# Performance work log

Hardware: AMD Instinct MI355X
Metric: run time of the kernel (lower is better)

Reference implementation:

```python
import jax, jax.numpy as jnp
import numpy as np

PS = 32768        # bag size (num patches)
D_IN = 1024       # input feature dim (hardcoded Linear(1024,512))
D = 512           # mlp_dim
D_ATT = 128       # DAttention hidden dim (ABMIL D)
N_CLS = 2
MASK_RATIO_H = 0.5
K_MASK = int(np.ceil(PS * MASK_RATIO_H))   # high-attention patches masked out
LEN_KEEP = PS - K_MASK                     # static keep length


def setup_inputs() -> dict:
    key = jax.random.key(0)
    ks = jax.random.split(key, 8)
    n = lambda i, shp, sc: jax.random.normal(ks[i], shp, dtype=jnp.float32) * sc
    return {
        "x": n(0, (1, PS, D_IN), 1.0),
        "attn": jax.random.uniform(ks[1], (1, PS), dtype=jnp.float32),
        "teacher_cls_feat": n(2, (1, D), 1.0),
        # patch_to_emb: Linear(1024,512) + ReLU (xavier-ish init)
        "W_emb": n(3, (D_IN, D), 0.03), "b_emb": jnp.zeros((D,), jnp.float32),
        # DAttention score net: Linear(512,128) -> GELU -> Linear(128,1)
        "W_a1": n(4, (D, D_ATT), 0.06), "b_a1": jnp.zeros((D_ATT,), jnp.float32),
        "W_a2": n(5, (D_ATT, 1), 0.12), "b_a2": jnp.zeros((1,), jnp.float32),
        # predictor: Linear(512, n_classes)
        "W_pred": n(6, (D, N_CLS), 0.06), "b_pred": jnp.zeros((N_CLS,), jnp.float32),
    }


def _keep_ids(attn_1d):
    # select_mask_fn(largest=True, mask_ratio=0.5, random_ratio=1.0, select_inv=False):
    # top-k highest-attention indices are MASKED; keep = set-difference complement.
    _, top_idx = jax.lax.top_k(attn_1d, K_MASK)
    masked = jnp.zeros((PS,), dtype=bool).at[top_idx].set(True)
    # complement in ascending order (matches set(range(ps)).difference iteration)
    return jnp.nonzero(~masked, size=LEN_KEEP, fill_value=0)[0]


def reference(x, attn, teacher_cls_feat, W_emb, b_emb, W_a1, b_a1, W_a2, b_a2,
              W_pred, b_pred):
    # patch_to_emb + ReLU  (dropout=0 -> identity)
    h = jax.nn.relu(jnp.einsum("bnd,de->bne", x, W_emb) + b_emb)   # [1,PS,512]

    keep = _keep_ids(attn[0])                                        # [LEN_KEEP]
    hk = h[:, keep, :]                                               # [1,LK,512]

    # DAttention pooling: scores -> softmax over kept instances -> weighted sum
    s = jax.nn.gelu(jnp.einsum("bnd,dk->bnk", hk, W_a1) + b_a1, approximate=False)
    s = (jnp.einsum("bnk,ko->bno", s, W_a2) + b_a2)[..., 0]          # [1,LK]
    A = jax.nn.softmax(s, axis=-1)
    feat = jnp.einsum("bn,bnd->bd", A, hk)                           # [1,512]

    logit = feat @ W_pred + b_pred                                   # [1,2]

    # SoftTargetCrossEntropy_v2 between student bag feature and (detached) teacher
    t = jax.lax.stop_gradient(teacher_cls_feat)
    cls_loss = jnp.mean(jnp.sum(
        -jax.nn.softmax(t, axis=-1) * jax.nn.log_softmax(feat, axis=-1), axis=-1))

    return logit, cls_loss
```

## Files before the change

### kernel.cpp

```cpp
#include <hip/hip_runtime.h>
#include <hip/hip_bf16.h>
#include <math.h>

#define PS    32768
#define DIN   1024
#define DMID  512
#define DATT  128
#define KMASK 16384
#define LKEEP 16384

typedef unsigned short u16;
typedef __attribute__((ext_vector_type(8))) short short8;
typedef __attribute__((ext_vector_type(4))) float f32x4;

__device__ __forceinline__ u16 f2bf(float f){
  unsigned x = __float_as_uint(f);
  unsigned r = (x + 0x7fffu + ((x >> 16) & 1u)) >> 16;
  return (u16)r;
}
__device__ __forceinline__ u16 f2bf_hw(float f){
  __hip_bfloat16 h = __float2bfloat16(f);
  return *reinterpret_cast<u16*>(&h);
}
__device__ __forceinline__ float bf2f(u16 u){
  return __uint_as_float(((unsigned)u) << 16);
}
__device__ __forceinline__ unsigned fkey(float f){
  unsigned b = __float_as_uint(f);
  return (b & 0x80000000u) ? ~b : (b | 0x80000000u);
}

#define GLDS16(g,l) __builtin_amdgcn_global_load_lds( \
    (const __attribute__((address_space(1))) void*)(g), \
    (__attribute__((address_space(3))) void*)(l), 16, 0, 0)

#define MEMPIN() asm volatile("" ::: "memory")

__global__ __launch_bounds__(1024) void k_head(const float* __restrict__ attn,
                                               int* __restrict__ keep_ids,
                                               const float* __restrict__ Wemb,
                                               u16* __restrict__ wet,
                                               const float* __restrict__ Wa1,
                                               u16* __restrict__ wa1t){
  __shared__ int histL[16384];
  __shared__ int suf[1024];
  __shared__ unsigned ck[4096];
  __shared__ int ci[4096];
  __shared__ float tile[4][32][33];
  __shared__ int sh_B, sh_kp, cnt;
  __shared__ unsigned sh_C;
  __shared__ int sh_thr;
  __shared__ int wbase[16];
  __shared__ int sh_base;
  const int t = threadIdx.x, b = blockIdx.x;

  if (b >= 32){
    const int grp = t >> 8, ts = t & 255;
    const int ob = (b - 32) * 4 + grp;
    const int tx = ts & 31, ty = ts >> 5;
    if (ob < 512){
      const int c0 = (ob & 15) * 32, r0 = (ob >> 4) * 32;
      for (int i = 0; i < 32; i += 8)
        tile[grp][ty + i][tx] = Wemb[(size_t)(r0 + ty + i) * DMID + c0 + tx];
      __syncthreads();
      for (int i = 0; i < 32; i += 8)
        wet[(size_t)(c0 + ty + i) * DIN + r0 + tx] = f2bf(tile[grp][tx][ty + i]);
    } else {
      const int b2 = ob - 512;
      const int c0 = (b2 & 3) * 32, r0 = (b2 >> 2) * 32;
      for (int i = 0; i < 32; i += 8)
        tile[grp][ty + i][tx] = Wa1[(size_t)(r0 + ty + i) * DATT + c0 + tx];
      __syncthreads();
      for (int i = 0; i < 32; i += 8)
        wa1t[(size_t)(c0 + ty + i) * DMID + r0 + tx] = f2bf(tile[grp][tx][ty + i]);
    }
    return;
  }

  for (int i = t; i < 16384; i += 1024) histL[i] = 0;
  __syncthreads();
  for (int i = t; i < PS; i += 1024)
    atomicAdd(&histL[fkey(attn[i]) >> 18], 1);
  __syncthreads();

  int local[16]; int s = 0;
  const int base = t * 16;
  for (int j = 0; j < 16; j++){ local[j] = histL[base + j]; s += local[j]; }
  suf[t] = s; __syncthreads();
  for (int off = 1; off < 1024; off <<= 1){
    int v = (t + off < 1024) ? suf[t + off] : 0;
    __syncthreads();
    suf[t] += v;
    __syncthreads();
  }
  const int above = (t < 1023) ? suf[t + 1] : 0;
  if (above < KMASK && KMASK <= suf[t]){
    int cum = above;
    for (int bb = 15; bb >= 0; bb--){
      int c = local[bb];
      if (cum + c >= KMASK){ sh_B = base + bb; sh_kp = KMASK - cum; break; }
      cum += c;
    }
  }
  if (t == 0) cnt = 0;
  __syncthreads();
  const unsigned B = (unsigned)sh_B;
  const int kp = sh_kp;

  for (int i = t; i < PS; i += 1024){
    unsigned u = fkey(attn[i]);
    if ((u >> 18) == B){
      int p = atomicAdd(&cnt, 1);
      if (p < 4096){ ck[p] = u; ci[p] = i; }
    }
  }
  __syncthreads();
  int n = cnt; if (n > 4096) n = 4096;
  for (int p = t; p < n; p += 1024){
    const unsigned mk = ck[p]; const int mi = ci[p];
    int rank = 0;
    for (int j = 0; j < n; j++){
      const unsigned kj = ck[j];
      rank += (kj > mk) || (kj == mk && ci[j] < mi);
    }
    if (rank == kp - 1){ sh_C = mk; sh_thr = mi; }
  }
  __syncthreads();
  const unsigned C = sh_C;
  const int thr = sh_thr;

  const int i = b * 1024 + t;
  const unsigned u = fkey(attn[i]);
  const bool kept = (u < C) || (u == C && i > thr);
  const unsigned long long bal = __ballot(kept);
  const int lane = t & 63, w = t >> 6;
  if (lane == 0) wbase[w] = __popcll(bal);
  int cnt2 = 0;
  for (int j = t; j < b * 1024; j += 1024){
    const unsigned u2 = fkey(attn[j]);
    cnt2 += (u2 < C) || (u2 == C && j > thr);
  }
  suf[t] = cnt2; __syncthreads();
  for (int st = 512; st > 0; st >>= 1){ if (t < st) suf[t] += suf[t + st]; __syncthreads(); }
  if (t == 0){
    sh_base = suf[0];
    int run = 0;
    for (int j = 0; j < 16; j++){ int c = wbase[j]; wbase[j] = run; run += c; }
  }
  __syncthreads();
  if (kept){
    const int lr = __popcll(bal & ((1ull << lane) - 1ull));
    keep_ids[sh_base + wbase[w] + lr] = i;
  }
}

__global__ __launch_bounds__(512) void k_gemm1g(const float* __restrict__ xg,
                                                const int* __restrict__ keep,
                                                const u16* __restrict__ wet,
                                                const float* __restrict__ bemb,
                                                u16* __restrict__ hbf){
  __shared__ __align__(16) u16 As[2][128 * 32];
  __shared__ __align__(16) u16 Bs[2][128 * 32];
  const int t = threadIdx.x;
  const int wid = t >> 6, lane = t & 63;
  const int g = lane >> 4, li = lane & 15;
  const int m_ = blockIdx.x;
  const int by = (m_ & 7) + 8 * (m_ >> 5);
  const int bx = (m_ >> 3) & 3;
  const int brow = by * 128, bcol = bx * 128;
  const int wrow0 = (wid >> 2) * 64, wcol0 = (wid & 3) * 32;

  f32x4 acc[4][2];
  for (int mm = 0; mm < 4; mm++)
    for (int nn = 0; nn < 2; nn++)
      acc[mm][nn] = (f32x4){0.f, 0.f, 0.f, 0.f};

  const int rsub = t >> 2, q8 = (t & 3) * 8;
  const float* gA = xg + (size_t)keep[brow + rsub] * DIN + q8;
  const int r4 = lane >> 2, cB = lane & 3;
  const u16* gB = wet + ((size_t)(bcol + wid * 16 + r4) * DIN + cB * 8);

#define CVT_STORE(dstbuf, lo, hi) { \
    short8 pk_; \
    pk_[0] = (short)f2bf_hw((lo).x); pk_[1] = (short)f2bf_hw((lo).y); \
    pk_[2] = (short)f2bf_hw((lo).z); pk_[3] = (short)f2bf_hw((lo).w); \
    pk_[4] = (short)f2bf_hw((hi).x); pk_[5] = (short)f2bf_hw((hi).y); \
    pk_[6] = (short)f2bf_hw((hi).z); pk_[7] = (short)f2bf_hw((hi).w); \
    *(short8*)&As[dstbuf][rsub * 32 + q8] = pk_; }

#define READ_MFMA(cur) { \
    short8 a_[4], b_[2]; \
    _Pragma("unroll") \
    for (int mm = 0; mm < 4; mm++) \
      a_[mm] = *(const short8*)&As[cur][(wrow0 + mm * 16 + li) * 32 + g * 8]; \
    _Pragma("unroll") \
    for (int nn = 0; nn < 2; nn++) \
      b_[nn] = *(const short8*)&Bs[cur][(wcol0 + nn * 16 + li) * 32 + g * 8]; \
    for (int mm = 0; mm < 4; mm++) \
      for (int nn = 0; nn < 2; nn++) \
        acc[mm][nn] = __builtin_amdgcn_mfma_f32_16x16x32_bf16(a_[mm], b_[nn], acc[mm][nn], 0, 0, 0); }

  float4 a0lo = *(const float4*)(gA);
  float4 a0hi = *(const float4*)(gA + 4);
  MEMPIN();
  GLDS16(gB, &Bs[0][wid * 512]);
  MEMPIN();
  float4 avlo = *(const float4*)(gA + 32);
  float4 avhi = *(const float4*)(gA + 36);
  MEMPIN();
  CVT_STORE(0, a0lo, a0hi);
  asm volatile("s_waitcnt vmcnt(2) lgkmcnt(0)" ::: "memory");
  __builtin_amdgcn_s_barrier();

#pragma unroll 2
  for (int k = 0; k < 30; k++){
    const int cur = k & 1, nxt = cur ^ 1;
    GLDS16(gB + (k + 1) * 32, &Bs[nxt][wid * 512]);
    MEMPIN();
    float4 nvlo = *(const float4*)(gA + (k + 2) * 32);
    float4 nvhi = *(const float4*)(gA + (k + 2) * 32 + 4);
    asm volatile("s_waitcnt vmcnt(5)" ::: "memory");
    READ_MFMA(cur);
    MEMPIN();
    CVT_STORE(nxt, avlo, avhi);
    avlo = nvlo; avhi = nvhi;
    asm volatile("s_waitcnt lgkmcnt(0)" ::: "memory");
    __builtin_amdgcn_s_barrier();
  }
  {
    GLDS16(gB + 31 * 32, &Bs[1][wid * 512]);
    asm volatile("s_waitcnt vmcnt(3)" ::: "memory");
    READ_MFMA(0);
    MEMPIN();
    CVT_STORE(1, avlo, avhi);
    asm volatile("s_waitcnt lgkmcnt(0)" ::: "memory");
    __builtin_amdgcn_s_barrier();
  }
  {
    asm volatile("s_waitcnt vmcnt(0)" ::: "memory");
    READ_MFMA(1);
  }
#undef CVT_STORE
#undef READ_MFMA

  for (int nn = 0; nn < 2; nn++){
    const int col = bcol + wcol0 + nn * 16 + li;
    const float be = bemb[col];
    for (int mm = 0; mm < 4; mm++){
      const int row0 = brow + wrow0 + mm * 16 + g * 4;
      f32x4 v = acc[mm][nn];
      for (int r = 0; r < 4; r++){
        float val = v[r] + be;
        if (val < 0.f) val = 0.f;
        hbf[(size_t)(row0 + r) * DMID + col] = f2bf(val);
      }
    }
  }
}

__global__ __launch_bounds__(256) void k_gemm2(const u16* __restrict__ hbf,
                                               const u16* __restrict__ wa1t,
                                               const float* __restrict__ ba1,
                                               const float* __restrict__ wa2,
                                               const float* __restrict__ ba2,
                                               float* __restrict__ s_out,
                                               float* __restrict__ smax,
                                               float* __restrict__ ssum,
                                               float* __restrict__ partial){
  __shared__ __align__(16) u16 As[64 * 32];
  __shared__ __align__(16) u16 Bs[128 * 32];
  __shared__ float p_lds[64];
  __shared__ float sh_m;
  const int t = threadIdx.x;
  const int wid = t >> 6, lane = t & 63;
  const int g = lane >> 4, li = lane & 15;
  const int brow = blockIdx.x * 64;
  const int wrow0 = (wid >> 1) * 32, wcol0 = (wid & 1) * 64;

  f32x4 acc[2][4];
  for (int m = 0; m < 2; m++)
    for (int n = 0; n < 4; n++)
      acc[m][n] = (f32x4){0.f, 0.f, 0.f, 0.f};

  const int r4 = lane >> 2, c4 = lane & 3;
  const u16* gA = hbf  + ((size_t)(brow + wid * 16 + r4) * DMID + c4 * 8);
  const u16* gB = wa1t + ((size_t)(wid * 32 + r4) * DMID + c4 * 8);
  u16* lA = As + wid * 512;
  u16* lB = Bs + wid * 1024;

  for (int k0 = 0; k0 < DMID; k0 += 32){
    GLDS16(gA + k0,             lA);
    GLDS16(gB + k0,             lB);
    GLDS16(gB + 16 * DMID + k0, lB + 512);
    __syncthreads();
    short8 a[2], b[4];
    for (int m = 0; m < 2; m++)
      a[m] = *(const short8*)&As[(wrow0 + m * 16 + li) * 32 + g * 8];
    for (int n = 0; n < 4; n++)
      b[n] = *(const short8*)&Bs[(wcol0 + n * 16 + li) * 32 + g * 8];
    for (int m = 0; m < 2; m++)
      for (int n = 0; n < 4; n++)
        acc[m][n] = __builtin_amdgcn_mfma_f32_16x16x32_bf16(a[m], b[n], acc[m][n], 0, 0, 0);
    __syncthreads();
  }

  float rsum[2][4] = {{0.f,0.f,0.f,0.f},{0.f,0.f,0.f,0.f}};
  for (int n = 0; n < 4; n++){
    const int col = wcol0 + n * 16 + li;
    const float b1 = ba1[col], w2 = wa2[col];
    for (int m = 0; m < 2; m++){
      f32x4 v = acc[m][n];
      for (int r = 0; r < 4; r++){
        float xv = v[r] + b1;
        float ge = 0.5f * xv * (1.0f + erff(xv * 0.70710678118654752f));
        rsum[m][r] += ge * w2;
      }
    }
  }
  const float bb = ba2[0];
  for (int m = 0; m < 2; m++){
    for (int r = 0; r < 4; r++){
      float v = rsum[m][r];
      v += __shfl_xor(v, 1); v += __shfl_xor(v, 2);
      v += __shfl_xor(v, 4); v += __shfl_xor(v, 8);
      if (li == 0) s_out[brow + wrow0 + m * 16 + g * 4 + r] = v + bb;
    }
  }
  __syncthreads();
  if (t < 64){
    const float sv = s_out[brow + t];
    float mx = sv;
    for (int off = 1; off < 64; off <<= 1) mx = fmaxf(mx, __shfl_xor(mx, off));
    float ez = expf(sv - mx);
    for (int off = 1; off < 64; off <<= 1) ez += __shfl_xor(ez, off);
    if (t == 0){ smax[blockIdx.x] = mx; ssum[blockIdx.x] = ez; sh_m = mx; }
  }
  __syncthreads();
  if (t < 64) p_lds[t] = expf(s_out[brow + t] - sh_m);
  __syncthreads();
  {
    const int d0 = t * 2;
    float v0 = 0.f, v1 = 0.f;
    for (int j = 0; j < 64; j++){
      const float pj = p_lds[j];
      const unsigned hv = *(const unsigned*)&hbf[(size_t)(brow + j) * DMID + d0];
      v0 += pj * bf2f((u16)(hv & 0xffffu));
      v1 += pj * bf2f((u16)(hv >> 16));
    }
    partial[(size_t)blockIdx.x * DMID + d0]     = v0;
    partial[(size_t)blockIdx.x * DMID + d0 + 1] = v1;
  }
}

__global__ __launch_bounds__(512) void k_final(const float* __restrict__ partial,
                                               const float* __restrict__ smax,
                                               const float* __restrict__ ssum,
                                               const float* __restrict__ teach,
                                               const float* __restrict__ Wp,
                                               const float* __restrict__ bp,
                                               float* __restrict__ out){
  __shared__ float red[512];
  __shared__ float coef[256];
  const int t = threadIdx.x;

  red[t] = (t < 256) ? smax[t] : -INFINITY; __syncthreads();
  for (int st = 256; st > 0; st >>= 1){ if (t < st) red[t] = fmaxf(red[t], red[t + st]); __syncthreads(); }
  const float m_s = red[0]; __syncthreads();
  if (t < 256) coef[t] = expf(smax[t] - m_s);
  __syncthreads();
  red[t] = (t < 256) ? ssum[t] * coef[t] : 0.f; __syncthreads();
  for (int st = 256; st > 0; st >>= 1){ if (t < st) red[t] += red[t + st]; __syncthreads(); }
  const float invZ = 1.0f / red[0]; __syncthreads();

  float f = 0.f;
  for (int b = 0; b < 256; b++) f += partial[(size_t)b * DMID + t] * coef[b];
  f *= invZ;
  const float td = teach[t];

  red[t] = f; __syncthreads();
  for (int st = 256; st > 0; st >>= 1){ if (t < st) red[t] = fmaxf(red[t], red[t + st]); __syncthreads(); }
  const float mf = red[0]; __syncthreads();

  red[t] = td; __syncthreads();
  for (int st = 256; st > 0; st >>= 1){ if (t < st) red[t] = fmaxf(red[t], red[t + st]); __syncthreads(); }
  const float mt = red[0]; __syncthreads();

  red[t] = expf(f - mf); __syncthreads();
  for (int st = 256; st > 0; st >>= 1){ if (t < st) red[t] += red[t + st]; __syncthreads(); }
  const float Zf = red[0]; __syncthreads();

  const float pt = expf(td - mt);
  red[t] = pt; __syncthreads();
  for (int st = 256; st > 0; st >>= 1){ if (t < st) red[t] += red[t + st]; __syncthreads(); }
  const float Zt = red[0]; __syncthreads();

  red[t] = pt * f; __syncthreads();
  for (int st = 256; st > 0; st >>= 1){ if (t < st) red[t] += red[t + st]; __syncthreads(); }
  const float S1 = red[0]; __syncthreads();

  red[t] = f * Wp[t * 2 + 0]; __syncthreads();
  for (int st = 256; st > 0; st >>= 1){ if (t < st) red[t] += red[t + st]; __syncthreads(); }
  const float L0 = red[0]; __syncthreads();

  red[t] = f * Wp[t * 2 + 1]; __syncthreads();
  for (int st = 256; st > 0; st >>= 1){ if (t < st) red[t] += red[t + st]; __syncthreads(); }
  const float L1 = red[0];

  if (t == 0){
    out[0] = L0 + bp[0];
    out[1] = L1 + bp[1];
    out[2] = (mf + logf(Zf)) - S1 / Zt;
  }
}

extern "C" void kernel_launch(void* const* d_in, const int* in_sizes, int n_in,
                              void* d_out, int out_size, void* d_ws, size_t ws_size,
                              hipStream_t stream){
  const float* x     = (const float*)d_in[0];
  const float* attn  = (const float*)d_in[1];
  const float* teach = (const float*)d_in[2];
  const float* Wemb  = (const float*)d_in[3];
  const float* bemb  = (const float*)d_in[4];
  const float* Wa1   = (const float*)d_in[5];
  const float* ba1   = (const float*)d_in[6];
  const float* Wa2   = (const float*)d_in[7];
  const float* ba2   = (const float*)d_in[8];
  const float* Wp    = (const float*)d_in[9];
  const float* bp    = (const float*)d_in[10];
  float* out = (float*)d_out;

  char* ws = (char*)d_ws;
  int*   keep = (int*)(ws + 0);
  float* s    = (float*)(ws + 65536);
  float* smax = (float*)(ws + 131072);
  float* ssum = (float*)(ws + 132096);
  u16*   wet  = (u16*)(ws + 200704);
  u16*   wa1t = (u16*)(ws + 200704 + 1048576);
  float* partial = (float*)(ws + 200704 + 1048576 + 131072);
  u16*   hbf  = (u16*)(ws + 200704 + 1048576 + 131072 + 33554432);

  k_head<<<dim3(176), dim3(1024), 0, stream>>>(attn, keep, Wemb, wet, Wa1, wa1t);
  k_gemm1g<<<dim3(512), dim3(512), 0, stream>>>(x, keep, wet, bemb, hbf);
  k_gemm2<<<dim3(LKEEP / 64), dim3(256), 0, stream>>>(hbf, wa1t, ba1, Wa2, ba2, s, smax, ssum, partial);
  k_final<<<dim3(1), dim3(512), 0, stream>>>(partial, smax, ssum, teach, Wp, bp, out);
}
```

Before: 107.6 us.

## Split gather-convert into its own kernel and triple-buffer GEMM1 with direct LDS loads

The fused gather+fp32→bf16 conversion in the first GEMM is moved into a separate gather kernel that writes a compact bf16 copy of the kept rows. The GEMM then loads both A and B tiles with global-to-LDS loads through a three-stage buffer ring, dropping the register conversion and per-iteration LDS stores. This removes conversion work from the MFMA loop and deepens the prefetch. In exchange it adds an extra kernel launch and a 32 MB bf16 write plus read-back, and the partial buffer now aliases the xbf region.

```diff
diff --git a/kernel.cpp b/kernel.cpp
--- a/kernel.cpp
+++ b/kernel.cpp
@@ -154,13 +154,29 @@
   }
 }
 
-__global__ __launch_bounds__(512) void k_gemm1g(const float* __restrict__ xg,
+__global__ __launch_bounds__(256) void k_gather(const float* __restrict__ x,
                                                 const int* __restrict__ keep,
-                                                const u16* __restrict__ wet,
-                                                const float* __restrict__ bemb,
-                                                u16* __restrict__ hbf){
-  __shared__ __align__(16) u16 As[2][128 * 32];
-  __shared__ __align__(16) u16 Bs[2][128 * 32];
+                                                u16* __restrict__ xbf){
+  const int t = threadIdx.x;
+  const int j0 = blockIdx.x * 4;
+#pragma unroll
+  for (int r = 0; r < 4; r++){
+    const int j = j0 + r;
+    const int id = keep[j];
+    const float4 v = ((const float4*)(x + (size_t)id * DIN))[t];
+    ushort4 pk;
+    pk.x = f2bf_hw(v.x); pk.y = f2bf_hw(v.y);
+    pk.z = f2bf_hw(v.z); pk.w = f2bf_hw(v.w);
+    ((ushort4*)(xbf + (size_t)j * DIN))[t] = pk;
+  }
+}
+
+__global__ __launch_bounds__(512) void k_gemm1(const u16* __restrict__ xbf,
+                                               const u16* __restrict__ wet,
+                                               const float* __restrict__ bemb,
+                                               u16* __restrict__ hbf){
+  __shared__ __align__(16) u16 As[3][128 * 32];
+  __shared__ __align__(16) u16 Bs[3][128 * 32];
   const int t = threadIdx.x;
   const int wid = t >> 6, lane = t & 63;
   const int g = lane >> 4, li = lane & 15;
@@ -175,18 +191,9 @@
     for (int nn = 0; nn < 2; nn++)
       acc[mm][nn] = (f32x4){0.f, 0.f, 0.f, 0.f};
 
-  const int rsub = t >> 2, q8 = (t & 3) * 8;
-  const float* gA = xg + (size_t)keep[brow + rsub] * DIN + q8;
-  const int r4 = lane >> 2, cB = lane & 3;
-  const u16* gB = wet + ((size_t)(bcol + wid * 16 + r4) * DIN + cB * 8);
-
-#define CVT_STORE(dstbuf, lo, hi) { \
-    short8 pk_; \
-    pk_[0] = (short)f2bf_hw((lo).x); pk_[1] = (short)f2bf_hw((lo).y); \
-    pk_[2] = (short)f2bf_hw((lo).z); pk_[3] = (short)f2bf_hw((lo).w); \
-    pk_[4] = (short)f2bf_hw((hi).x); pk_[5] = (short)f2bf_hw((hi).y); \
-    pk_[6] = (short)f2bf_hw((hi).z); pk_[7] = (short)f2bf_hw((hi).w); \
-    *(short8*)&As[dstbuf][rsub * 32 + q8] = pk_; }
+  const int r4 = lane >> 2, c4 = lane & 3;
+  const u16* gA = xbf + ((size_t)(brow + wid * 16 + r4) * DIN + c4 * 8);
+  const u16* gB = wet + ((size_t)(bcol + wid * 16 + r4) * DIN + c4 * 8);
 
 #define READ_MFMA(cur) { \
     short8 a_[4], b_[2]; \
@@ -200,47 +207,29 @@
       for (int nn = 0; nn < 2; nn++) \
         acc[mm][nn] = __builtin_amdgcn_mfma_f32_16x16x32_bf16(a_[mm], b_[nn], acc[mm][nn], 0, 0, 0); }
 
-  float4 a0lo = *(const float4*)(gA);
-  float4 a0hi = *(const float4*)(gA + 4);
+  GLDS16(gA,      &As[0][wid * 512]);
+  GLDS16(gB,      &Bs[0][wid * 512]);
   MEMPIN();
-  GLDS16(gB, &Bs[0][wid * 512]);
+  GLDS16(gA + 32, &As[1][wid * 512]);
+  GLDS16(gB + 32, &Bs[1][wid * 512]);
   MEMPIN();
-  float4 avlo = *(const float4*)(gA + 32);
-  float4 avhi = *(const float4*)(gA + 36);
-  MEMPIN();
-  CVT_STORE(0, a0lo, a0hi);
-  asm volatile("s_waitcnt vmcnt(2) lgkmcnt(0)" ::: "memory");
+
+#pragma unroll 3
+  for (int k = 0; k < 30; k++){
+    asm volatile("s_waitcnt vmcnt(2)" ::: "memory");
+    __builtin_amdgcn_s_barrier();
+    READ_MFMA(k % 3);
+    MEMPIN();
+    GLDS16(gA + (k + 2) * 32, &As[(k + 2) % 3][wid * 512]);
+    GLDS16(gB + (k + 2) * 32, &Bs[(k + 2) % 3][wid * 512]);
+    MEMPIN();
+  }
+  asm volatile("s_waitcnt vmcnt(2)" ::: "memory");
   __builtin_amdgcn_s_barrier();
-
-#pragma unroll 2
-  for (int k = 0; k < 30; k++){
-    const int cur = k & 1, nxt = cur ^ 1;
-    GLDS16(gB + (k + 1) * 32, &Bs[nxt][wid * 512]);
-    MEMPIN();
-    float4 nvlo = *(const float4*)(gA + (k + 2) * 32);
-    float4 nvhi = *(const float4*)(gA + (k + 2) * 32 + 4);
-    asm volatile("s_waitcnt vmcnt(5)" ::: "memory");
-    READ_MFMA(cur);
-    MEMPIN();
-    CVT_STORE(nxt, avlo, avhi);
-    avlo = nvlo; avhi = nvhi;
-    asm volatile("s_waitcnt lgkmcnt(0)" ::: "memory");
-    __builtin_amdgcn_s_barrier();
-  }
-  {
-    GLDS16(gB + 31 * 32, &Bs[1][wid * 512]);
-    asm volatile("s_waitcnt vmcnt(3)" ::: "memory");
-    READ_MFMA(0);
-    MEMPIN();
-    CVT_STORE(1, avlo, avhi);
-    asm volatile("s_waitcnt lgkmcnt(0)" ::: "memory");
-    __builtin_amdgcn_s_barrier();
-  }
-  {
-    asm volatile("s_waitcnt vmcnt(0)" ::: "memory");
-    READ_MFMA(1);
-  }
-#undef CVT_STORE
+  READ_MFMA(0);
+  asm volatile("s_waitcnt vmcnt(0)" ::: "memory");
+  __builtin_amdgcn_s_barrier();
+  READ_MFMA(1);
 #undef READ_MFMA
 
   for (int nn = 0; nn < 2; nn++){
@@ -436,11 +425,13 @@
   float* ssum = (float*)(ws + 132096);
   u16*   wet  = (u16*)(ws + 200704);
   u16*   wa1t = (u16*)(ws + 200704 + 1048576);
-  float* partial = (float*)(ws + 200704 + 1048576 + 131072);
-  u16*   hbf  = (u16*)(ws + 200704 + 1048576 + 131072 + 33554432);
+  u16*   xbf  = (u16*)(ws + 1380352);
+  float* partial = (float*)xbf;
+  u16*   hbf  = (u16*)(ws + 34934784);
 
   k_head<<<dim3(176), dim3(1024), 0, stream>>>(attn, keep, Wemb, wet, Wa1, wa1t);
-  k_gemm1g<<<dim3(512), dim3(512), 0, stream>>>(x, keep, wet, bemb, hbf);
+  k_gather<<<dim3(4096), dim3(256), 0, stream>>>(x, keep, xbf);
+  k_gemm1<<<dim3(512), dim3(512), 0, stream>>>(xbf, wet, bemb, hbf);
   k_gemm2<<<dim3(LKEEP / 64), dim3(256), 0, stream>>>(hbf, wa1t, ba1, Wa2, ba2, s, smax, ssum, partial);
   k_final<<<dim3(1), dim3(512), 0, stream>>>(partial, smax, ssum, teach, Wp, bp, out);
 }
```

After: 115.9 us. 1.08x slower.
